# Optimization experiments

Measured on AMD Instinct MI355X. Metric: run time of the kernel, lower is better.

The kernel has to match this reference:

```python
import jax, jax.numpy as jnp
import numpy as np

EPS = 1e-5
K = 3

def _bn(x, g, b):
    # training-mode BatchNorm2d: batch stats over (N,H,W), biased variance
    m = jnp.mean(x, axis=(0, 2, 3), keepdims=True)
    v = jnp.var(x, axis=(0, 2, 3), keepdims=True)
    return (x - m) * jax.lax.rsqrt(v + EPS) * g[None, :, None, None] + b[None, :, None, None]

def _gelu(x):
    return jax.nn.gelu(x, approximate=False)

def _dyn_dw(x, aw1, ab1, aw2, ab2):
    # dynamic depthwise conv: per-sample k^2 softmax weights shared over channels
    b, c, h, w = x.shape
    gap = jnp.mean(x, axis=(2, 3))                              # (b,c)
    h1 = jax.nn.relu(jnp.einsum('oc,bc->bo', aw1, gap) + ab1)   # (b,c//8)
    kw = jax.nn.softmax(jnp.einsum('oc,bc->bo', aw2, h1) + ab2, axis=1)  # (b,k^2)
    xp = jnp.pad(x, ((0, 0), (0, 0), (1, 1), (1, 1)))
    out = jnp.zeros_like(x)
    idx = 0
    for i in range(K):
        for j in range(K):
            out = out + kw[:, idx, None, None, None] * xp[:, :, i:i + h, j:j + w]
            idx += 1
    return out

def _channel_att(x, w1, w2):
    avg = jnp.mean(x, axis=(2, 3))        # (b,C)
    mx = jnp.max(x, axis=(2, 3))          # (b,C)
    def fc(v):
        return jnp.einsum('oc,bc->bo', w2, jax.nn.relu(jnp.einsum('oc,bc->bo', w1, v)))
    s = jax.nn.sigmoid(fc(avg) + fc(mx))  # (b,C)
    return s[:, :, None, None] * x

def _forward(x, w1, b1, g1, be1, aw1, ab1, aw2, ab2, g2, be2,
             ca_w1, ca_w2, pw, pb, g3, be3, sw, sb):
    b, n, d = x.shape
    h = w = int(np.sqrt(n))
    residual = x
    xi = jnp.transpose(x.reshape(b, h, w, d), (0, 3, 1, 2))       # (b,d,h,w)
    # pw_expand: 1x1 conv -> GELU -> BN
    y = jnp.einsum('oc,bchw->bohw', w1, xi) + b1[None, :, None, None]
    y = _bn(_gelu(y), g1, be1)                                    # (b,4d,h,w)
    # dw_conv: dynamic depthwise -> GELU -> BN -> channel attention
    y = _dyn_dw(y, aw1, ab1, aw2, ab2)
    y = _bn(_gelu(y), g2, be2)
    y = _channel_att(y, ca_w1, ca_w2)
    # spatial attention
    avg_o = jnp.mean(y, axis=1, keepdims=True)
    max_o = jnp.max(y, axis=1, keepdims=True)
    sp_in = jnp.concatenate([avg_o, max_o], axis=1)               # (b,2,h,w)
    sp = jax.lax.conv_general_dilated(sp_in, sw, (1, 1), ((3, 3), (3, 3)),
                                      dimension_numbers=('NCHW', 'OIHW', 'NCHW'))
    sp = jax.nn.sigmoid(sp + sb[None, :, None, None])
    y = y * sp
    # pw_project: 1x1 conv -> BN
    y = jnp.einsum('oc,bchw->bohw', pw, y) + pb[None, :, None, None]
    y = _bn(y, g3, be3)
    y = jnp.transpose(y, (0, 2, 3, 1)).reshape(b, n, d)
    return residual + y

def setup_inputs() -> dict:
    key = jax.random.key(0)
    ks = jax.random.split(key, 16)
    d, C = 256, 1024
    def rn(k, shape, fan):
        return jax.random.normal(k, shape, jnp.float32) * np.float32(np.sqrt(2.0 / fan))
    return {
        'x': jax.random.normal(ks[0], (8, 1024, d), jnp.float32),
        'w1': rn(ks[1], (C, d), d), 'b1': jnp.zeros((C,), jnp.float32),
        'g1': jnp.ones((C,), jnp.float32), 'be1': jnp.zeros((C,), jnp.float32),
        'aw1': rn(ks[2], (C // 8, C), C), 'ab1': jnp.zeros((C // 8,), jnp.float32),
        'aw2': rn(ks[3], (K * K, C // 8), C // 8), 'ab2': jnp.zeros((K * K,), jnp.float32),
        'g2': jnp.ones((C,), jnp.float32), 'be2': jnp.zeros((C,), jnp.float32),
        'ca_w1': rn(ks[4], (C // 16, C), C), 'ca_w2': rn(ks[5], (C, C // 16), C // 16),
        'pw': rn(ks[6], (d, C), C), 'pb': jnp.zeros((d,), jnp.float32),
        'g3': jnp.ones((d,), jnp.float32), 'be3': jnp.zeros((d,), jnp.float32),
        'sw': rn(ks[7], (1, 2, 7, 7), 2 * 49), 'sb': jnp.zeros((1,), jnp.float32),
    }

def reference(x, w1, b1, g1, be1, aw1, ab1, aw2, ab2, g2, be2,
              ca_w1, ca_w2, pw, pb, g3, be3, sw, sb):
    return _forward(x, w1, b1, g1, be1, aw1, ab1, aw2, ab2, g2, be2,
                    ca_w1, ca_w2, pw, pb, g3, be3, sw, sb)
```

## Files before the change

kernel.cpp:

```cpp
#include <hip/hip_runtime.h>
#include <math.h>

constexpr int B = 8;
constexpr int D = 256;
constexpr int C = 1024;
constexpr int H = 32, W = 32;
constexpr int P = H * W;
constexpr int M = B * P;
constexpr float EPS = 1e-5f;

typedef unsigned short u16;
typedef unsigned int u32;
typedef __attribute__((ext_vector_type(8))) short short8;
typedef __attribute__((ext_vector_type(4))) float floatx4;

constexpr size_t WS_CHSUM1 = 0;
constexpr size_t WS_CHSQ1  = 1024;
constexpr size_t WS_GAPSUM = 2048;
constexpr size_t WS_CHSUM3 = 10240;
constexpr size_t WS_CHSQ3  = 10496;
constexpr size_t WS_ACC_COUNT = 10752;
constexpr size_t WS_SCALE1 = 11264;
constexpr size_t WS_SHIFT1 = 12288;
constexpr size_t WS_KW     = 21504;
constexpr size_t WS_SCALE2 = 21760;
constexpr size_t WS_SHIFT2 = 22784;
constexpr size_t WS_AVGBN  = 23808;
constexpr size_t WS_MXBN   = 32000;
constexpr size_t WS_SATT   = 40192;
constexpr size_t WS_AVGO   = 48384;
constexpr size_t WS_MAXO   = 56576;
constexpr size_t WS_SP     = 64768;
constexpr size_t WS_PSUM2  = 73728;
constexpr size_t WS_PSQ2   = 335872;
constexpr size_t WS_PMAX2  = 598016;
constexpr size_t WS_PMIN2  = 860160;
constexpr size_t WS_PRE    = 1122304;
constexpr size_t WS_T1B    = 3219456;
constexpr size_t WS_T2B    = 7413760;
constexpr size_t WS_XB     = 11608064;
constexpr size_t WS_W1B    = 12656640;
constexpr size_t WS_PWB    = 12787712;
constexpr size_t WS_YB     = 12918784;

__device__ __forceinline__ float gelu_exact(float v) {
    return 0.5f * v * (1.0f + erff(v * 0.70710678118654752440f));
}

__device__ __forceinline__ u16 f2bf(float f) {
    u32 u = __float_as_uint(f);
    u += 0x7fff + ((u >> 16) & 1);
    return (u16)(u >> 16);
}

__device__ __forceinline__ float bf2f(u16 v) {
    return __uint_as_float(((u32)v) << 16);
}

__global__ __launch_bounds__(256) void cvt_all_kernel(const float* __restrict__ x,
                                                      const float* __restrict__ w1,
                                                      const float* __restrict__ pw,
                                                      u16* __restrict__ xb,
                                                      u16* __restrict__ w1b,
                                                      u16* __restrict__ pwb) {
    const int i = blockIdx.x * 256 + threadIdx.x;
    const float* src;
    u16* dst;
    int off;
    if (i < 524288)      { src = x;  dst = xb;  off = i; }
    else if (i < 589824) { src = w1; dst = w1b; off = i - 524288; }
    else                 { src = pw; dst = pwb; off = i - 589824; }
    const float4 v = *(const float4*)(src + (size_t)off * 4);
    uint2 o;
    o.x = ((u32)f2bf(v.x)) | ((u32)f2bf(v.y) << 16);
    o.y = ((u32)f2bf(v.z)) | ((u32)f2bf(v.w) << 16);
    *(uint2*)(dst + (size_t)off * 4) = o;
}

template<int KD, int EPI, int NS, int MB, int NB>
__global__ __launch_bounds__(256) void mfma_gemm_kernel(
    const u16* __restrict__ A,
    const u16* __restrict__ Bw,
    const float* __restrict__ bias,
    const float* __restrict__ rowscale,
    void* __restrict__ outv,
    float* __restrict__ csum,
    float* __restrict__ csq,
    float* __restrict__ gsum)
{
    constexpr int MI = MB / 32;
    constexpr int NJ = NB / 32;
    extern __shared__ u16 smem[];
    u16* As = smem;
    u16* Bs = smem + MB * 32;
    const int t = threadIdx.x;
    const int lane = t & 63;
    const int row0 = blockIdx.y * MB;
    const int col0 = blockIdx.x * NB;
    const int wv = t >> 6;
    const int wrow = (wv >> 1) * (MB / 2);
    const int wcol = (wv & 1) * (NB / 2);
    const int lm = lane & 15;
    const int lk8 = (lane >> 4) * 8;

    const int srow = t >> 2;
    const int scol = (t & 3) * 8;

    const u16* gA0 = A + (size_t)(row0 + srow) * KD + scol;
    const u16* gA1 = A + (size_t)(row0 + 64 + srow) * KD + scol;
    const u16* gB0 = Bw + (size_t)(col0 + srow) * KD + scol;

    const floatx4 zero = {0.f, 0.f, 0.f, 0.f};
    floatx4 acc[MI][NJ];
#pragma unroll
    for (int i = 0; i < MI; ++i)
#pragma unroll
        for (int j = 0; j < NJ; ++j) acc[i][j] = zero;

    for (int k0 = 0; k0 < KD; k0 += 32) {
        __builtin_amdgcn_global_load_lds(
            (const __attribute__((address_space(1))) void*)(gA0 + k0),
            (__attribute__((address_space(3))) void*)(As + t * 8), 16, 0, 0);
        if (MB == 128)
            __builtin_amdgcn_global_load_lds(
                (const __attribute__((address_space(1))) void*)(gA1 + k0),
                (__attribute__((address_space(3))) void*)(As + 2048 + t * 8), 16, 0, 0);
        __builtin_amdgcn_global_load_lds(
            (const __attribute__((address_space(1))) void*)(gB0 + k0),
            (__attribute__((address_space(3))) void*)(Bs + t * 8), 16, 0, 0);
        __syncthreads();
        short8 af[MI], bf[NJ];
#pragma unroll
        for (int i = 0; i < MI; ++i)
            af[i] = *(const short8*)(As + (wrow + i * 16 + lm) * 32 + lk8);
#pragma unroll
        for (int j = 0; j < NJ; ++j)
            bf[j] = *(const short8*)(Bs + (wcol + j * 16 + lm) * 32 + lk8);
#pragma unroll
        for (int i = 0; i < MI; ++i)
#pragma unroll
            for (int j = 0; j < NJ; ++j)
                acc[i][j] = __builtin_amdgcn_mfma_f32_16x16x32_bf16(af[i], bf[j], acc[i][j], 0, 0, 0);
        __syncthreads();
    }

    float colsum[NJ], colsq[NJ];
#pragma unroll
    for (int j = 0; j < NJ; ++j) { colsum[j] = 0.f; colsq[j] = 0.f; }

    if (EPI == 0) {
        u16* Cs = smem;
#pragma unroll
        for (int i = 0; i < MI; ++i) {
#pragma unroll
            for (int r = 0; r < 4; ++r) {
                const int lrow = wrow + i * 16 + (lane >> 4) * 4 + r;
#pragma unroll
                for (int j = 0; j < NJ; ++j) {
                    const int lcol = wcol + j * 16 + lm;
                    const float tv = gelu_exact(acc[i][j][r] + bias[col0 + lcol]);
                    Cs[lrow * NB + lcol] = f2bf(tv);
                    colsum[j] += tv;
                    colsq[j] = fmaf(tv, tv, colsq[j]);
                }
            }
        }
        __syncthreads();
        const int rr = t >> 1;
        const int hh = (t & 1) * 32;
        u16* outp = (u16*)outv + (size_t)(row0 + rr) * NS + col0 + hh;
#pragma unroll
        for (int k = 0; k < 4; ++k) {
            *(uint4*)(outp + k * 8) = *(const uint4*)(Cs + rr * NB + hh + k * 8);
        }
    } else {
#pragma unroll
        for (int i = 0; i < MI; ++i) {
#pragma unroll
            for (int r = 0; r < 4; ++r) {
                const int grow = row0 + wrow + i * 16 + (lane >> 4) * 4 + r;
                const float rs = rowscale[grow];
#pragma unroll
                for (int j = 0; j < NJ; ++j) {
                    const int gcol = col0 + wcol + j * 16 + lm;
                    const float tv = rs * acc[i][j][r] + bias[gcol];
                    ((float*)outv)[(size_t)grow * NS + gcol] = tv;
                    colsum[j] += tv;
                    colsq[j] = fmaf(tv, tv, colsq[j]);
                }
            }
        }
    }

    const int bb = (blockIdx.y * MB) >> 10;
#pragma unroll
    for (int j = 0; j < NJ; ++j) {
        float s = colsum[j];
        float q = colsq[j];
        s += __shfl_xor(s, 16); s += __shfl_xor(s, 32);
        q += __shfl_xor(q, 16); q += __shfl_xor(q, 32);
        if (lane < 16) {
            const int c = col0 + wcol + j * 16 + lm;
            atomicAdd(&csum[c], s);
            atomicAdd(&csq[c], q);
            if (EPI == 0) atomicAdd(&gsum[bb * NS + c], s);
        }
    }
}

__global__ __launch_bounds__(1024) void dynmlp_kernel(const float* __restrict__ chsum1,
                                                      const float* __restrict__ chsq1,
                                                      const float* __restrict__ gapsum,
                                                      const float* __restrict__ g1,
                                                      const float* __restrict__ be1,
                                                      const float* __restrict__ aw1,
                                                      const float* __restrict__ ab1,
                                                      const float* __restrict__ aw2,
                                                      const float* __restrict__ ab2,
                                                      float* __restrict__ scale1,
                                                      float* __restrict__ shift1,
                                                      float* __restrict__ kw) {
    const int b = blockIdx.x;
    const int t = threadIdx.x;
    const int wave = t >> 6, lane = t & 63;
    __shared__ float g[1024];
    __shared__ float h1[128];
    __shared__ float logits[12];
    {
        const float m = chsum1[t] * (1.0f / (float)M);
        const float var = chsq1[t] * (1.0f / (float)M) - m * m;
        const float rstd = rsqrtf(var + EPS);
        const float sc = rstd * g1[t];
        const float sh = be1[t] - m * sc;
        if (b == 0) { scale1[t] = sc; shift1[t] = sh; }
        g[t] = gapsum[b * C + t] * (1.0f / (float)P) * sc + sh;
    }
    __syncthreads();
#pragma unroll
    for (int k = 0; k < 8; ++k) {
        const int u = wave * 8 + k;
        const float4* wr = (const float4*)(aw1 + (size_t)u * C);
        float s = 0.f;
#pragma unroll
        for (int ch = 0; ch < 4; ++ch) {
            const float4 wv = wr[lane + 64 * ch];
            const float4 sv = *(const float4*)(g + 4 * lane + 256 * ch);
            s += wv.x * sv.x + wv.y * sv.y + wv.z * sv.z + wv.w * sv.w;
        }
#pragma unroll
        for (int off = 1; off < 64; off <<= 1) s += __shfl_xor(s, off);
        if (lane == 0) h1[u] = fmaxf(s + ab1[u], 0.f);
    }
    __syncthreads();
    if (wave < 9) {
        float s = aw2[wave * 128 + lane] * h1[lane]
                + aw2[wave * 128 + 64 + lane] * h1[64 + lane];
#pragma unroll
        for (int off = 1; off < 64; off <<= 1) s += __shfl_xor(s, off);
        if (lane == 0) logits[wave] = s + ab2[wave];
    }
    __syncthreads();
    if (t == 0) {
        float mx = logits[0];
        for (int i = 1; i < 9; ++i) mx = fmaxf(mx, logits[i]);
        float e[9], den = 0.f;
        for (int i = 0; i < 9; ++i) { e[i] = expf(logits[i] - mx); den += e[i]; }
        const float inv = 1.0f / den;
        for (int i = 0; i < 9; ++i) kw[b * 9 + i] = e[i] * inv;
    }
}

__global__ __launch_bounds__(256) void dwconv_kernel(const u16* __restrict__ t1b,
                                                     const float* __restrict__ scale1,
                                                     const float* __restrict__ shift1,
                                                     const float* __restrict__ kw,
                                                     u16* __restrict__ t2b,
                                                     float* __restrict__ psum,
                                                     float* __restrict__ psq,
                                                     float* __restrict__ pmax,
                                                     float* __restrict__ pmin) {
    const int b = blockIdx.y >> 5;
    const int h = blockIdx.y & 31;
    const int c0 = (blockIdx.x * 256 + threadIdx.x) * 2;
    float k[9];
#pragma unroll
    for (int i = 0; i < 9; ++i) k[i] = kw[b * 9 + i];
    const float sc0 = scale1[c0],     sh0 = shift1[c0];
    const float sc1 = scale1[c0 + 1], sh1 = shift1[c0 + 1];
    const u16* base = t1b + (size_t)b * P * C + c0;
    const bool rok[3] = { h > 0, true, h < H - 1 };

    float2 win[3][3];
    const float2 z = {0.f, 0.f};
#pragma unroll
    for (int ri = 0; ri < 3; ++ri) {
        win[ri][0] = z;
#pragma unroll
        for (int ci = 1; ci < 3; ++ci) {
            if (rok[ri]) {
                const u32 v = *(const u32*)(base + ((size_t)((h + ri - 1) * W + (ci - 1))) * C);
                float2 r;
                r.x = fmaf(bf2f((u16)(v & 0xffff)), sc0, sh0);
                r.y = fmaf(bf2f((u16)(v >> 16)),    sc1, sh1);
                win[ri][ci] = r;
            } else win[ri][ci] = z;
        }
    }

    float s0 = 0.f, q0 = 0.f, mx0 = -INFINITY, mn0 = INFINITY;
    float s1 = 0.f, q1 = 0.f, mx1 = -INFINITY, mn1 = INFINITY;
    for (int w = 0; w < W; ++w) {
        float a0 = 0.f, a1 = 0.f;
#pragma unroll
        for (int ri = 0; ri < 3; ++ri)
#pragma unroll
            for (int ci = 0; ci < 3; ++ci) {
                a0 = fmaf(k[ri * 3 + ci], win[ri][ci].x, a0);
                a1 = fmaf(k[ri * 3 + ci], win[ri][ci].y, a1);
            }
        const float y0 = gelu_exact(a0);
        const float y1 = gelu_exact(a1);
        *(u32*)(t2b + ((size_t)b * P + h * W + w) * C + c0) =
            ((u32)f2bf(y0)) | ((u32)f2bf(y1) << 16);
        s0 += y0; q0 = fmaf(y0, y0, q0); mx0 = fmaxf(mx0, y0); mn0 = fminf(mn0, y0);
        s1 += y1; q1 = fmaf(y1, y1, q1); mx1 = fmaxf(mx1, y1); mn1 = fminf(mn1, y1);
        if (w < W - 1) {
#pragma unroll
            for (int ri = 0; ri < 3; ++ri) {
                win[ri][0] = win[ri][1];
                win[ri][1] = win[ri][2];
                if (rok[ri] && (w + 2 < W)) {
                    const u32 v = *(const u32*)(base + ((size_t)((h + ri - 1) * W + (w + 2))) * C);
                    float2 r;
                    r.x = fmaf(bf2f((u16)(v & 0xffff)), sc0, sh0);
                    r.y = fmaf(bf2f((u16)(v >> 16)),    sc1, sh1);
                    win[ri][2] = r;
                } else win[ri][2] = z;
            }
        }
    }
    const int idx = b * 32 + h;
    psum[c0 * 256 + idx] = s0;  psum[(c0 + 1) * 256 + idx] = s1;
    psq [c0 * 256 + idx] = q0;  psq [(c0 + 1) * 256 + idx] = q1;
    pmax[c0 * 256 + idx] = mx0; pmax[(c0 + 1) * 256 + idx] = mx1;
    pmin[c0 * 256 + idx] = mn0; pmin[(c0 + 1) * 256 + idx] = mn1;
}

__global__ __launch_bounds__(256) void stats2_kernel(const float* __restrict__ psum,
                                                     const float* __restrict__ psq,
                                                     const float* __restrict__ pmax,
                                                     const float* __restrict__ pmin,
                                                     const float* __restrict__ g2,
                                                     const float* __restrict__ be2,
                                                     float* __restrict__ scale2,
                                                     float* __restrict__ shift2,
                                                     float* __restrict__ avgbn,
                                                     float* __restrict__ mxbn) {
    const int c = blockIdx.x;
    const int t = threadIdx.x;
    const int base = c * 256 + t;
    float s  = psum[base];
    float q  = psq[base];
    float mx = pmax[base];
    float mn = pmin[base];
#pragma unroll
    for (int off = 1; off < 32; off <<= 1) {
        s += __shfl_xor(s, off);
        q += __shfl_xor(q, off);
        mx = fmaxf(mx, __shfl_xor(mx, off));
        mn = fminf(mn, __shfl_xor(mn, off));
    }
    __shared__ float bs[8], bq[8], bmx[8], bmn[8];
    __shared__ float sc_sh[2];
    if ((t & 31) == 0) {
        const int b = t >> 5;
        bs[b] = s; bq[b] = q; bmx[b] = mx; bmn[b] = mn;
    }
    __syncthreads();
    if (t == 0) {
        float S = 0.f, Q = 0.f;
#pragma unroll
        for (int b = 0; b < 8; ++b) { S += bs[b]; Q += bq[b]; }
        const float m = S * (1.0f / (float)M);
        const float var = Q * (1.0f / (float)M) - m * m;
        const float rstd = rsqrtf(var + EPS);
        const float sc = rstd * g2[c];
        const float sh = be2[c] - m * sc;
        scale2[c] = sc;
        shift2[c] = sh;
        sc_sh[0] = sc; sc_sh[1] = sh;
    }
    __syncthreads();
    if (t < 8) {
        const float sc = sc_sh[0], sh = sc_sh[1];
        avgbn[t * C + c] = bs[t] * (1.0f / (float)P) * sc + sh;
        mxbn[t * C + c] = (sc >= 0.f ? bmx[t] : bmn[t]) * sc + sh;
    }
}

__global__ __launch_bounds__(1024) void chatt_kernel(const float* __restrict__ avgbn,
                                                     const float* __restrict__ mxbn,
                                                     const float* __restrict__ caw1,
                                                     const float* __restrict__ caw2,
                                                     float* __restrict__ s_att) {
    const int b = blockIdx.x;
    const int t = threadIdx.x;
    const int wave = t >> 6, lane = t & 63;
    __shared__ float la[1024], lx[1024], ha[64], hm[64];
    la[t] = avgbn[b * C + t];
    lx[t] = mxbn[b * C + t];
    __syncthreads();
#pragma unroll
    for (int k = 0; k < 8; ++k) {
        const int u = wave * 8 + k;
        const int row = u & 63;
        const float* src = (u < 64) ? la : lx;
        const float4* wr = (const float4*)(caw1 + (size_t)row * C);
        float s = 0.f;
#pragma unroll
        for (int ch = 0; ch < 4; ++ch) {
            const float4 wv = wr[lane + 64 * ch];
            const float4 sv = *(const float4*)(src + 4 * lane + 256 * ch);
            s += wv.x * sv.x + wv.y * sv.y + wv.z * sv.z + wv.w * sv.w;
        }
#pragma unroll
        for (int off = 1; off < 64; off <<= 1) s += __shfl_xor(s, off);
        if (lane == 0) {
            s = fmaxf(s, 0.f);
            if (u < 64) ha[row] = s; else hm[row] = s;
        }
    }
    __syncthreads();
    {
        const float4* w2 = (const float4*)(caw2 + (size_t)t * 64);
        float s = 0.f;
#pragma unroll
        for (int j = 0; j < 16; ++j) {
            const float4 wv = w2[j];
            s += wv.x * (ha[j * 4 + 0] + hm[j * 4 + 0]);
            s += wv.y * (ha[j * 4 + 1] + hm[j * 4 + 1]);
            s += wv.z * (ha[j * 4 + 2] + hm[j * 4 + 2]);
            s += wv.w * (ha[j * 4 + 3] + hm[j * 4 + 3]);
        }
        s_att[b * C + t] = 1.0f / (1.0f + expf(-s));
    }
}

__global__ __launch_bounds__(256) void yq_kernel(const u16* __restrict__ t2b,
                                                 const float* __restrict__ scale2,
                                                 const float* __restrict__ shift2,
                                                 const float* __restrict__ s_att,
                                                 u16* __restrict__ yb,
                                                 float* __restrict__ avg_o,
                                                 float* __restrict__ max_o) {
    const int row = blockIdx.x;
    const int b = row >> 10;
    const int t = threadIdx.x;
    const int c0 = t * 4;
    const uint2 vv = *(const uint2*)(t2b + (size_t)row * C + c0);
    const float v0 = bf2f((u16)(vv.x & 0xffff));
    const float v1 = bf2f((u16)(vv.x >> 16));
    const float v2 = bf2f((u16)(vv.y & 0xffff));
    const float v3 = bf2f((u16)(vv.y >> 16));
    const float4 sc = *(const float4*)(scale2 + c0);
    const float4 sh = *(const float4*)(shift2 + c0);
    const float4 sa = *(const float4*)(s_att + (size_t)b * C + c0);
    const float y0 = fmaf(v0, sc.x, sh.x) * sa.x;
    const float y1 = fmaf(v1, sc.y, sh.y) * sa.y;
    const float y2 = fmaf(v2, sc.z, sh.z) * sa.z;
    const float y3 = fmaf(v3, sc.w, sh.w) * sa.w;
    uint2 o;
    o.x = ((u32)f2bf(y0)) | ((u32)f2bf(y1) << 16);
    o.y = ((u32)f2bf(y2)) | ((u32)f2bf(y3) << 16);
    *(uint2*)(yb + (size_t)row * C + c0) = o;
    float s = (y0 + y1) + (y2 + y3);
    float mx = fmaxf(fmaxf(y0, y1), fmaxf(y2, y3));
#pragma unroll
    for (int off = 32; off > 0; off >>= 1) {
        s += __shfl_down(s, off);
        mx = fmaxf(mx, __shfl_down(mx, off));
    }
    __shared__ float ss[4], sm[4];
    const int wave = t >> 6, lane = t & 63;
    if (lane == 0) { ss[wave] = s; sm[wave] = mx; }
    __syncthreads();
    if (t == 0) {
        const float S = ss[0] + ss[1] + ss[2] + ss[3];
        const float Mx = fmaxf(fmaxf(sm[0], sm[1]), fmaxf(sm[2], sm[3]));
        avg_o[row] = S * (1.0f / (float)C);
        max_o[row] = Mx;
    }
}

__global__ __launch_bounds__(1024) void spconv_kernel(const float* __restrict__ avg_o,
                                                      const float* __restrict__ max_o,
                                                      const float* __restrict__ sw,
                                                      const float* __restrict__ sb,
                                                      float* __restrict__ sp) {
    const int b = blockIdx.x;
    const int t = threadIdx.x;
    __shared__ float pa[P], pm[P], wsh[98];
    pa[t] = avg_o[b * P + t];
    pm[t] = max_o[b * P + t];
    if (t < 98) wsh[t] = sw[t];
    const float sbv = sb[0];
    __syncthreads();
    const int h = t >> 5, w = t & 31;
    float acc = sbv;
#pragma unroll
    for (int i = 0; i < 7; ++i) {
        const int hh = h + i - 3;
        if (hh < 0 || hh >= H) continue;
#pragma unroll
        for (int j = 0; j < 7; ++j) {
            const int ww = w + j - 3;
            if (ww < 0 || ww >= W) continue;
            const int pidx = hh * W + ww;
            acc = fmaf(wsh[i * 7 + j], pa[pidx], acc);
            acc = fmaf(wsh[49 + i * 7 + j], pm[pidx], acc);
        }
    }
    sp[b * P + t] = 1.0f / (1.0f + expf(-acc));
}

__global__ __launch_bounds__(256) void final_kernel(const float* __restrict__ x,
                                                    const float* __restrict__ pre,
                                                    const float* __restrict__ chsum3,
                                                    const float* __restrict__ chsq3,
                                                    const float* __restrict__ g3,
                                                    const float* __restrict__ be3,
                                                    float* __restrict__ out) {
    __shared__ float lsc[256], lsh[256];
    const int t = threadIdx.x;
    {
        const float m = chsum3[t] * (1.0f / (float)M);
        const float var = chsq3[t] * (1.0f / (float)M) - m * m;
        const float rstd = rsqrtf(var + EPS);
        const float sc = rstd * g3[t];
        lsc[t] = sc;
        lsh[t] = be3[t] - m * sc;
    }
    __syncthreads();
    const int i = blockIdx.x * 256 + t;
    const int e = i * 4;
    const int d = e & 255;
    const float4 xv = *(const float4*)(x + e);
    const float4 pv = *(const float4*)(pre + e);
    const float4 sc = *(const float4*)(lsc + d);
    const float4 sh = *(const float4*)(lsh + d);
    float4 o;
    o.x = xv.x + fmaf(pv.x, sc.x, sh.x);
    o.y = xv.y + fmaf(pv.y, sc.y, sh.y);
    o.z = xv.z + fmaf(pv.z, sc.z, sh.z);
    o.w = xv.w + fmaf(pv.w, sc.w, sh.w);
    *(float4*)(out + e) = o;
}

extern "C" void kernel_launch(void* const* d_in, const int* in_sizes, int n_in,
                              void* d_out, int out_size, void* d_ws, size_t ws_size,
                              hipStream_t stream) {
    const float* x    = (const float*)d_in[0];
    const float* w1   = (const float*)d_in[1];
    const float* b1   = (const float*)d_in[2];
    const float* g1   = (const float*)d_in[3];
    const float* be1  = (const float*)d_in[4];
    const float* aw1  = (const float*)d_in[5];
    const float* ab1  = (const float*)d_in[6];
    const float* aw2  = (const float*)d_in[7];
    const float* ab2  = (const float*)d_in[8];
    const float* g2   = (const float*)d_in[9];
    const float* be2  = (const float*)d_in[10];
    const float* caw1 = (const float*)d_in[11];
    const float* caw2 = (const float*)d_in[12];
    const float* pw   = (const float*)d_in[13];
    const float* pb   = (const float*)d_in[14];
    const float* g3   = (const float*)d_in[15];
    const float* be3  = (const float*)d_in[16];
    const float* sw   = (const float*)d_in[17];
    const float* sb   = (const float*)d_in[18];
    float* out = (float*)d_out;
    float* ws = (float*)d_ws;

    hipMemsetAsync(ws, 0, WS_ACC_COUNT * sizeof(float), stream);

    float* chsum1  = ws + WS_CHSUM1;
    float* chsq1   = ws + WS_CHSQ1;
    float* gapsum  = ws + WS_GAPSUM;
    float* chsum3  = ws + WS_CHSUM3;
    float* chsq3   = ws + WS_CHSQ3;
    float* scale1  = ws + WS_SCALE1;
    float* shift1  = ws + WS_SHIFT1;
    float* kw      = ws + WS_KW;
    float* scale2  = ws + WS_SCALE2;
    float* shift2  = ws + WS_SHIFT2;
    float* avgbn   = ws + WS_AVGBN;
    float* mxbn    = ws + WS_MXBN;
    float* s_att   = ws + WS_SATT;
    float* avg_o   = ws + WS_AVGO;
    float* max_o   = ws + WS_MAXO;
    float* sp      = ws + WS_SP;
    float* psum2   = ws + WS_PSUM2;
    float* psq2    = ws + WS_PSQ2;
    float* pmax2   = ws + WS_PMAX2;
    float* pmin2   = ws + WS_PMIN2;
    float* pre     = ws + WS_PRE;
    u16* t1b = (u16*)(ws + WS_T1B);
    u16* t2b = (u16*)(ws + WS_T2B);
    u16* xb  = (u16*)(ws + WS_XB);
    u16* w1b = (u16*)(ws + WS_W1B);
    u16* pwb = (u16*)(ws + WS_PWB);
    u16* yb  = (u16*)(ws + WS_YB);

    cvt_all_kernel<<<dim3(2560), 256, 0, stream>>>(x, w1, pw, xb, w1b, pwb);
    mfma_gemm_kernel<256, 0, C, 128, 64><<<dim3(C / 64, M / 128), 256, 16384, stream>>>(
        xb, w1b, b1, nullptr, t1b, chsum1, chsq1, gapsum);
    dynmlp_kernel<<<dim3(B), 1024, 0, stream>>>(chsum1, chsq1, gapsum, g1, be1,
                                                aw1, ab1, aw2, ab2, scale1, shift1, kw);
    dwconv_kernel<<<dim3(C / 512, B * H), 256, 0, stream>>>(t1b, scale1, shift1, kw, t2b,
                                                            psum2, psq2, pmax2, pmin2);
    stats2_kernel<<<dim3(C), 256, 0, stream>>>(psum2, psq2, pmax2, pmin2, g2, be2,
                                               scale2, shift2, avgbn, mxbn);
    chatt_kernel<<<dim3(B), 1024, 0, stream>>>(avgbn, mxbn, caw1, caw2, s_att);
    yq_kernel<<<dim3(M), 256, 0, stream>>>(t2b, scale2, shift2, s_att, yb, avg_o, max_o);
    spconv_kernel<<<dim3(B), 1024, 0, stream>>>(avg_o, max_o, sw, sb, sp);
    mfma_gemm_kernel<1024, 1, D, 64, 64><<<dim3(D / 64, M / 64), 256, 8192, stream>>>(
        yb, pwb, pb, sp, pre, chsum3, chsq3, nullptr);
    final_kernel<<<dim3((M * D / 4) / 256), 256, 0, stream>>>(x, pre, chsum3, chsq3, g3, be3, out);
}
```

Before: 218.9 us.

## Fuse the whole pipeline into one persistent cooperative kernel with grid syncs

Adds a single cooperative mega-kernel of 512 blocks x 256 threads. It runs every stage in sequence, separated by grid-wide barriers: zeroing the workspace, bf16 conversion, the expand GEMM with GELU and statistics, the dynamic-weight MLP, the depthwise conv, BN2 finalisation, channel attention, the spatial reductions, the 7x7 conv, the projection GEMM, and the final BN plus residual. The aim is to remove per-kernel launch overhead, the separate memset and the gaps between the roughly ten kernels. In exchange, the small per-batch stages run on only 8 blocks while the rest of the grid waits, each grid.sync adds barrier latency, and the fixed grid size limits occupancy. The old multi-kernel path is kept as a fallback if the cooperative launch fails.

Result: slower. 808.0 us (+269.1%).

```diff
diff --git a/kernel.cpp b/kernel.cpp
--- a/kernel.cpp
+++ b/kernel.cpp
@@ -1,5 +1,8 @@
 #include <hip/hip_runtime.h>
+#include <hip/hip_cooperative_groups.h>
 #include <math.h>
+
+namespace cg = cooperative_groups;
 
 constexpr int B = 8;
 constexpr int D = 256;
@@ -57,6 +60,563 @@
     return __uint_as_float(((u32)v) << 16);
 }
 
+constexpr int NBLK = 512;
+constexpr int NTHR = 256;
+
+struct MegaParams {
+    const float *x, *w1, *b1, *g1, *be1, *aw1, *ab1, *aw2, *ab2, *g2, *be2,
+                *caw1, *caw2, *pw, *pb, *g3, *be3, *sw, *sb;
+    float* out;
+    float* ws;
+};
+
+__global__ __launch_bounds__(256, 2) void mega_kernel(MegaParams p) {
+    __shared__ __align__(16) u16 smu[8256];
+    float* smf = (float*)smu;
+
+    float* ws = p.ws;
+    float* chsum1 = ws + WS_CHSUM1;
+    float* chsq1  = ws + WS_CHSQ1;
+    float* gapsum = ws + WS_GAPSUM;
+    float* chsum3 = ws + WS_CHSUM3;
+    float* chsq3  = ws + WS_CHSQ3;
+    float* scale1 = ws + WS_SCALE1;
+    float* shift1 = ws + WS_SHIFT1;
+    float* kw     = ws + WS_KW;
+    float* scale2 = ws + WS_SCALE2;
+    float* shift2 = ws + WS_SHIFT2;
+    float* avgbn  = ws + WS_AVGBN;
+    float* mxbn   = ws + WS_MXBN;
+    float* s_att  = ws + WS_SATT;
+    float* avg_o  = ws + WS_AVGO;
+    float* max_o  = ws + WS_MAXO;
+    float* sp     = ws + WS_SP;
+    float* psum   = ws + WS_PSUM2;
+    float* psq    = ws + WS_PSQ2;
+    float* pmax   = ws + WS_PMAX2;
+    float* pmin   = ws + WS_PMIN2;
+    float* pre    = ws + WS_PRE;
+    u16* t1b = (u16*)(ws + WS_T1B);
+    u16* t2b = (u16*)(ws + WS_T2B);
+    u16* xb  = (u16*)(ws + WS_XB);
+    u16* w1b = (u16*)(ws + WS_W1B);
+    u16* pwb = (u16*)(ws + WS_PWB);
+    u16* yb  = (u16*)(ws + WS_YB);
+
+    cg::grid_group grid = cg::this_grid();
+    const int bid = blockIdx.x;
+    const int t = threadIdx.x;
+    const int lane = t & 63;
+    const int wave = t >> 6;
+    const int gtid = bid * NTHR + t;
+
+    for (int i = gtid; i < (int)WS_ACC_COUNT; i += NBLK * NTHR) ws[i] = 0.f;
+    for (int u = gtid; u < 655360; u += NBLK * NTHR) {
+        const float* src; u16* dst; int off;
+        if (u < 524288)      { src = p.x;  dst = xb;  off = u; }
+        else if (u < 589824) { src = p.w1; dst = w1b; off = u - 524288; }
+        else                 { src = p.pw; dst = pwb; off = u - 589824; }
+        const float4 v = *(const float4*)(src + (size_t)off * 4);
+        uint2 o;
+        o.x = ((u32)f2bf(v.x)) | ((u32)f2bf(v.y) << 16);
+        o.y = ((u32)f2bf(v.z)) | ((u32)f2bf(v.w) << 16);
+        *(uint2*)(dst + (size_t)off * 4) = o;
+    }
+    grid.sync();
+
+    {
+        u16* As = smu;
+        u16* Bs = smu + 4096;
+        u16* Cs = smu;
+        const int wrow = (wave >> 1) * 64;
+        const int wcol = (wave & 1) * 32;
+        const int lm = lane & 15;
+        const int lk8 = (lane >> 4) * 8;
+        const int srow = t >> 2;
+        const int scol = (t & 3) * 8;
+        for (int tile = bid; tile < 1024; tile += NBLK) {
+            const int row0 = (tile >> 4) * 128;
+            const int col0 = (tile & 15) * 64;
+            const u16* gA0 = xb + (size_t)(row0 + srow) * 256 + scol;
+            const u16* gA1 = xb + (size_t)(row0 + 64 + srow) * 256 + scol;
+            const u16* gB0 = w1b + (size_t)(col0 + srow) * 256 + scol;
+            const floatx4 zero = {0.f, 0.f, 0.f, 0.f};
+            floatx4 acc[4][2];
+#pragma unroll
+            for (int i = 0; i < 4; ++i) { acc[i][0] = zero; acc[i][1] = zero; }
+            for (int k0 = 0; k0 < 256; k0 += 32) {
+                __builtin_amdgcn_global_load_lds(
+                    (const __attribute__((address_space(1))) void*)(gA0 + k0),
+                    (__attribute__((address_space(3))) void*)(As + t * 8), 16, 0, 0);
+                __builtin_amdgcn_global_load_lds(
+                    (const __attribute__((address_space(1))) void*)(gA1 + k0),
+                    (__attribute__((address_space(3))) void*)(As + 2048 + t * 8), 16, 0, 0);
+                __builtin_amdgcn_global_load_lds(
+                    (const __attribute__((address_space(1))) void*)(gB0 + k0),
+                    (__attribute__((address_space(3))) void*)(Bs + t * 8), 16, 0, 0);
+                __syncthreads();
+                short8 af[4], bf[2];
+#pragma unroll
+                for (int i = 0; i < 4; ++i)
+                    af[i] = *(const short8*)(As + (wrow + i * 16 + lm) * 32 + lk8);
+#pragma unroll
+                for (int j = 0; j < 2; ++j)
+                    bf[j] = *(const short8*)(Bs + (wcol + j * 16 + lm) * 32 + lk8);
+#pragma unroll
+                for (int i = 0; i < 4; ++i)
+#pragma unroll
+                    for (int j = 0; j < 2; ++j)
+                        acc[i][j] = __builtin_amdgcn_mfma_f32_16x16x32_bf16(af[i], bf[j], acc[i][j], 0, 0, 0);
+                __syncthreads();
+            }
+            float colsum[2] = {0.f, 0.f}, colsq[2] = {0.f, 0.f};
+#pragma unroll
+            for (int i = 0; i < 4; ++i) {
+#pragma unroll
+                for (int r = 0; r < 4; ++r) {
+                    const int lrow = wrow + i * 16 + (lane >> 4) * 4 + r;
+#pragma unroll
+                    for (int j = 0; j < 2; ++j) {
+                        const int lcol = wcol + j * 16 + lm;
+                        const float tv = gelu_exact(acc[i][j][r] + p.b1[col0 + lcol]);
+                        Cs[lrow * 64 + lcol] = f2bf(tv);
+                        colsum[j] += tv;
+                        colsq[j] = fmaf(tv, tv, colsq[j]);
+                    }
+                }
+            }
+            __syncthreads();
+            {
+                const int rr = t >> 1;
+                const int hh = (t & 1) * 32;
+                u16* outp = t1b + (size_t)(row0 + rr) * C + col0 + hh;
+#pragma unroll
+                for (int k = 0; k < 4; ++k)
+                    *(uint4*)(outp + k * 8) = *(const uint4*)(Cs + rr * 64 + hh + k * 8);
+            }
+            const int bb = row0 >> 10;
+#pragma unroll
+            for (int j = 0; j < 2; ++j) {
+                float s = colsum[j];
+                float q = colsq[j];
+                s += __shfl_xor(s, 16); s += __shfl_xor(s, 32);
+                q += __shfl_xor(q, 16); q += __shfl_xor(q, 32);
+                if (lane < 16) {
+                    const int c = col0 + wcol + j * 16 + lm;
+                    atomicAdd(&chsum1[c], s);
+                    atomicAdd(&chsq1[c], q);
+                    atomicAdd(&gapsum[bb * C + c], s);
+                }
+            }
+            __syncthreads();
+        }
+    }
+    grid.sync();
+
+    if (bid < 8) {
+        const int b = bid;
+        float* g = smf;
+        float* h1 = smf + 1024;
+        float* logits = smf + 1152;
+#pragma unroll
+        for (int cc = 0; cc < 4; ++cc) {
+            const int c = t + 256 * cc;
+            const float m = chsum1[c] * (1.0f / (float)M);
+            const float var = chsq1[c] * (1.0f / (float)M) - m * m;
+            const float rstd = rsqrtf(var + EPS);
+            const float sc = rstd * p.g1[c];
+            const float sh = p.be1[c] - m * sc;
+            if (b == 0) { scale1[c] = sc; shift1[c] = sh; }
+            g[c] = gapsum[b * C + c] * (1.0f / (float)P) * sc + sh;
+        }
+        __syncthreads();
+        for (int k = 0; k < 32; ++k) {
+            const int u = wave * 32 + k;
+            const float4* wr = (const float4*)(p.aw1 + (size_t)u * C);
+            float s = 0.f;
+#pragma unroll
+            for (int ch = 0; ch < 4; ++ch) {
+                const float4 wv = wr[lane + 64 * ch];
+                const float4 sv = *(const float4*)(g + 4 * lane + 256 * ch);
+                s += wv.x * sv.x + wv.y * sv.y + wv.z * sv.z + wv.w * sv.w;
+            }
+#pragma unroll
+            for (int off = 1; off < 64; off <<= 1) s += __shfl_xor(s, off);
+            if (lane == 0) h1[u] = fmaxf(s + p.ab1[u], 0.f);
+        }
+        __syncthreads();
+        if (t < 9) {
+            float s = p.ab2[t];
+            for (int j = 0; j < 128; ++j) s = fmaf(p.aw2[t * 128 + j], h1[j], s);
+            logits[t] = s;
+        }
+        __syncthreads();
+        if (t == 0) {
+            float mx = logits[0];
+            for (int i = 1; i < 9; ++i) mx = fmaxf(mx, logits[i]);
+            float e[9], den = 0.f;
+            for (int i = 0; i < 9; ++i) { e[i] = expf(logits[i] - mx); den += e[i]; }
+            const float inv = 1.0f / den;
+            for (int i = 0; i < 9; ++i) kw[b * 9 + i] = e[i] * inv;
+        }
+    }
+    grid.sync();
+
+    {
+        const int cb = bid & 1;
+        const int bh = bid >> 1;
+        const int b = bh >> 5;
+        const int h = bh & 31;
+        const int c0 = (cb * 256 + t) * 2;
+        float k[9];
+#pragma unroll
+        for (int i = 0; i < 9; ++i) k[i] = kw[b * 9 + i];
+        const float sc0 = scale1[c0],     sh0 = shift1[c0];
+        const float sc1 = scale1[c0 + 1], sh1 = shift1[c0 + 1];
+        const u16* base = t1b + (size_t)b * P * C + c0;
+        const bool rok[3] = { h > 0, true, h < H - 1 };
+        float2 win[3][3];
+        const float2 z = {0.f, 0.f};
+#pragma unroll
+        for (int ri = 0; ri < 3; ++ri) {
+            win[ri][0] = z;
+#pragma unroll
+            for (int ci = 1; ci < 3; ++ci) {
+                if (rok[ri]) {
+                    const u32 v = *(const u32*)(base + ((size_t)((h + ri - 1) * W + (ci - 1))) * C);
+                    float2 r;
+                    r.x = fmaf(bf2f((u16)(v & 0xffff)), sc0, sh0);
+                    r.y = fmaf(bf2f((u16)(v >> 16)),    sc1, sh1);
+                    win[ri][ci] = r;
+                } else win[ri][ci] = z;
+            }
+        }
+        float s0 = 0.f, q0 = 0.f, mx0 = -INFINITY, mn0 = INFINITY;
+        float s1 = 0.f, q1 = 0.f, mx1 = -INFINITY, mn1 = INFINITY;
+        for (int w = 0; w < W; ++w) {
+            float a0 = 0.f, a1 = 0.f;
+#pragma unroll
+            for (int ri = 0; ri < 3; ++ri)
+#pragma unroll
+                for (int ci = 0; ci < 3; ++ci) {
+                    a0 = fmaf(k[ri * 3 + ci], win[ri][ci].x, a0);
+                    a1 = fmaf(k[ri * 3 + ci], win[ri][ci].y, a1);
+                }
+            const float y0 = gelu_exact(a0);
+            const float y1 = gelu_exact(a1);
+            *(u32*)(t2b + ((size_t)b * P + h * W + w) * C + c0) =
+                ((u32)f2bf(y0)) | ((u32)f2bf(y1) << 16);
+            s0 += y0; q0 = fmaf(y0, y0, q0); mx0 = fmaxf(mx0, y0); mn0 = fminf(mn0, y0);
+            s1 += y1; q1 = fmaf(y1, y1, q1); mx1 = fmaxf(mx1, y1); mn1 = fminf(mn1, y1);
+            if (w < W - 1) {
+#pragma unroll
+                for (int ri = 0; ri < 3; ++ri) {
+                    win[ri][0] = win[ri][1];
+                    win[ri][1] = win[ri][2];
+                    if (rok[ri] && (w + 2 < W)) {
+                        const u32 v = *(const u32*)(base + ((size_t)((h + ri - 1) * W + (w + 2))) * C);
+                        float2 r;
+                        r.x = fmaf(bf2f((u16)(v & 0xffff)), sc0, sh0);
+                        r.y = fmaf(bf2f((u16)(v >> 16)),    sc1, sh1);
+                        win[ri][2] = r;
+                    } else win[ri][2] = z;
+                }
+            }
+        }
+        const int idx = b * 32 + h;
+        psum[c0 * 256 + idx] = s0;  psum[(c0 + 1) * 256 + idx] = s1;
+        psq [c0 * 256 + idx] = q0;  psq [(c0 + 1) * 256 + idx] = q1;
+        pmax[c0 * 256 + idx] = mx0; pmax[(c0 + 1) * 256 + idx] = mx1;
+        pmin[c0 * 256 + idx] = mn0; pmin[(c0 + 1) * 256 + idx] = mn1;
+    }
+    grid.sync();
+
+    {
+        float* bs = smf;
+        float* bq = smf + 8;
+        float* bmx = smf + 16;
+        float* bmn = smf + 24;
+        float* sc_sh = smf + 32;
+        for (int c = bid; c < C; c += NBLK) {
+            const int base = c * 256 + t;
+            float s  = psum[base];
+            float q  = psq[base];
+            float mx = pmax[base];
+            float mn = pmin[base];
+#pragma unroll
+            for (int off = 1; off < 32; off <<= 1) {
+                s += __shfl_xor(s, off);
+                q += __shfl_xor(q, off);
+                mx = fmaxf(mx, __shfl_xor(mx, off));
+                mn = fminf(mn, __shfl_xor(mn, off));
+            }
+            if ((t & 31) == 0) {
+                const int b = t >> 5;
+                bs[b] = s; bq[b] = q; bmx[b] = mx; bmn[b] = mn;
+            }
+            __syncthreads();
+            if (t == 0) {
+                float S = 0.f, Q = 0.f;
+#pragma unroll
+                for (int b = 0; b < 8; ++b) { S += bs[b]; Q += bq[b]; }
+                const float m = S * (1.0f / (float)M);
+                const float var = Q * (1.0f / (float)M) - m * m;
+                const float rstd = rsqrtf(var + EPS);
+                const float sc = rstd * p.g2[c];
+                const float sh = p.be2[c] - m * sc;
+                scale2[c] = sc;
+                shift2[c] = sh;
+                sc_sh[0] = sc; sc_sh[1] = sh;
+            }
+            __syncthreads();
+            if (t < 8) {
+                const float sc = sc_sh[0], sh = sc_sh[1];
+                avgbn[t * C + c] = bs[t] * (1.0f / (float)P) * sc + sh;
+                mxbn[t * C + c] = (sc >= 0.f ? bmx[t] : bmn[t]) * sc + sh;
+            }
+            __syncthreads();
+        }
+    }
+    grid.sync();
+
+    if (bid < 8) {
+        const int b = bid;
+        float* la = smf;
+        float* lx = smf + 1024;
+        float* ha = smf + 2048;
+        float* hm = smf + 2112;
+#pragma unroll
+        for (int cc = 0; cc < 4; ++cc) {
+            const int c = t + 256 * cc;
+            la[c] = avgbn[b * C + c];
+            lx[c] = mxbn[b * C + c];
+        }
+        __syncthreads();
+        for (int k = 0; k < 32; ++k) {
+            const int u = wave * 32 + k;
+            const int row = u & 63;
+            const float* src = (u < 64) ? la : lx;
+            const float4* wr = (const float4*)(p.caw1 + (size_t)row * C);
+            float s = 0.f;
+#pragma unroll
+            for (int ch = 0; ch < 4; ++ch) {
+                const float4 wv = wr[lane + 64 * ch];
+                const float4 sv = *(const float4*)(src + 4 * lane + 256 * ch);
+                s += wv.x * sv.x + wv.y * sv.y + wv.z * sv.z + wv.w * sv.w;
+            }
+#pragma unroll
+            for (int off = 1; off < 64; off <<= 1) s += __shfl_xor(s, off);
+            if (lane == 0) {
+                s = fmaxf(s, 0.f);
+                if (u < 64) ha[row] = s; else hm[row] = s;
+            }
+        }
+        __syncthreads();
+#pragma unroll
+        for (int cc = 0; cc < 4; ++cc) {
+            const int c = t + 256 * cc;
+            const float4* w2 = (const float4*)(p.caw2 + (size_t)c * 64);
+            float s = 0.f;
+#pragma unroll
+            for (int j = 0; j < 16; ++j) {
+                const float4 wv = w2[j];
+                s += wv.x * (ha[j * 4 + 0] + hm[j * 4 + 0]);
+                s += wv.y * (ha[j * 4 + 1] + hm[j * 4 + 1]);
+                s += wv.z * (ha[j * 4 + 2] + hm[j * 4 + 2]);
+                s += wv.w * (ha[j * 4 + 3] + hm[j * 4 + 3]);
+            }
+            s_att[b * C + c] = 1.0f / (1.0f + expf(-s));
+        }
+    }
+    grid.sync();
+
+    {
+        const int gw = bid * 4 + wave;
+        for (int row = gw; row < M; row += NBLK * 4) {
+            const int b = row >> 10;
+            float s = 0.f, mx = -INFINITY;
+#pragma unroll
+            for (int cc = 0; cc < 4; ++cc) {
+                const int c0 = lane * 4 + 256 * cc;
+                const uint2 vv = *(const uint2*)(t2b + (size_t)row * C + c0);
+                const float v0 = bf2f((u16)(vv.x & 0xffff));
+                const float v1 = bf2f((u16)(vv.x >> 16));
+                const float v2 = bf2f((u16)(vv.y & 0xffff));
+                const float v3 = bf2f((u16)(vv.y >> 16));
+                const float4 sc = *(const float4*)(scale2 + c0);
+                const float4 sh = *(const float4*)(shift2 + c0);
+                const float4 sa = *(const float4*)(s_att + (size_t)b * C + c0);
+                const float y0 = fmaf(v0, sc.x, sh.x) * sa.x;
+                const float y1 = fmaf(v1, sc.y, sh.y) * sa.y;
+                const float y2 = fmaf(v2, sc.z, sh.z) * sa.z;
+                const float y3 = fmaf(v3, sc.w, sh.w) * sa.w;
+                uint2 o;
+                o.x = ((u32)f2bf(y0)) | ((u32)f2bf(y1) << 16);
+                o.y = ((u32)f2bf(y2)) | ((u32)f2bf(y3) << 16);
+                *(uint2*)(yb + (size_t)row * C + c0) = o;
+                s += (y0 + y1) + (y2 + y3);
+                mx = fmaxf(mx, fmaxf(fmaxf(y0, y1), fmaxf(y2, y3)));
+            }
+#pragma unroll
+            for (int off = 1; off < 64; off <<= 1) {
+                s += __shfl_xor(s, off);
+                mx = fmaxf(mx, __shfl_xor(mx, off));
+            }
+            if (lane == 0) {
+                avg_o[row] = s * (1.0f / (float)C);
+                max_o[row] = mx;
+            }
+        }
+    }
+    grid.sync();
+
+    if (bid < 8) {
+        const int b = bid;
+        float* pa = smf;
+        float* pm = smf + 1024;
+        float* wsh = smf + 2048;
+#pragma unroll
+        for (int cc = 0; cc < 4; ++cc) {
+            const int i = t + 256 * cc;
+            pa[i] = avg_o[b * P + i];
+            pm[i] = max_o[b * P + i];
+        }
+        if (t < 98) wsh[t] = p.sw[t];
+        const float sbv = p.sb[0];
+        __syncthreads();
+#pragma unroll
+        for (int cc = 0; cc < 4; ++cc) {
+            const int idx = t + 256 * cc;
+            const int h = idx >> 5, w = idx & 31;
+            float acc = sbv;
+#pragma unroll
+            for (int i = 0; i < 7; ++i) {
+                const int hh = h + i - 3;
+                if (hh < 0 || hh >= H) continue;
+#pragma unroll
+                for (int j = 0; j < 7; ++j) {
+                    const int ww = w + j - 3;
+                    if (ww < 0 || ww >= W) continue;
+                    const int pidx = hh * W + ww;
+                    acc = fmaf(wsh[i * 7 + j], pa[pidx], acc);
+                    acc = fmaf(wsh[49 + i * 7 + j], pm[pidx], acc);
+                }
+            }
+            sp[b * P + idx] = 1.0f / (1.0f + expf(-acc));
+        }
+    }
+    grid.sync();
+
+    {
+        u16* As = smu;
+        u16* Bs = smu + 2048;
+        float* Cs = smf;
+        const int wrow = (wave >> 1) * 32;
+        const int wcol = (wave & 1) * 32;
+        const int lm = lane & 15;
+        const int lk8 = (lane >> 4) * 8;
+        const int srow = t >> 2;
+        const int scol = (t & 3) * 8;
+        const int row0 = (bid >> 2) * 64;
+        const int col0 = (bid & 3) * 64;
+        const u16* gA0 = yb + (size_t)(row0 + srow) * C + scol;
+        const u16* gB0 = pwb + (size_t)(col0 + srow) * C + scol;
+        const floatx4 zero = {0.f, 0.f, 0.f, 0.f};
+        floatx4 acc[2][2];
+        acc[0][0] = zero; acc[0][1] = zero; acc[1][0] = zero; acc[1][1] = zero;
+        for (int k0 = 0; k0 < C; k0 += 32) {
+            __builtin_amdgcn_global_load_lds(
+                (const __attribute__((address_space(1))) void*)(gA0 + k0),
+                (__attribute__((address_space(3))) void*)(As + t * 8), 16, 0, 0);
+            __builtin_amdgcn_global_load_lds(
+                (const __attribute__((address_space(1))) void*)(gB0 + k0),
+                (__attribute__((address_space(3))) void*)(Bs + t * 8), 16, 0, 0);
+            __syncthreads();
+            short8 af[2], bf[2];
+#pragma unroll
+            for (int i = 0; i < 2; ++i)
+                af[i] = *(const short8*)(As + (wrow + i * 16 + lm) * 32 + lk8);
+#pragma unroll
+            for (int j = 0; j < 2; ++j)
+                bf[j] = *(const short8*)(Bs + (wcol + j * 16 + lm) * 32 + lk8);
+#pragma unroll
+            for (int i = 0; i < 2; ++i)
+#pragma unroll
+                for (int j = 0; j < 2; ++j)
+                    acc[i][j] = __builtin_amdgcn_mfma_f32_16x16x32_bf16(af[i], bf[j], acc[i][j], 0, 0, 0);
+            __syncthreads();
+        }
+        float colsum[2] = {0.f, 0.f}, colsq[2] = {0.f, 0.f};
+#pragma unroll
+        for (int i = 0; i < 2; ++i) {
+#pragma unroll
+            for (int r = 0; r < 4; ++r) {
+                const int lrow = wrow + i * 16 + (lane >> 4) * 4 + r;
+                const float rs = sp[row0 + lrow];
+#pragma unroll
+                for (int j = 0; j < 2; ++j) {
+                    const int lcol = wcol + j * 16 + lm;
+                    const float tv = rs * acc[i][j][r] + p.pb[col0 + lcol];
+                    Cs[lrow * 64 + lcol] = tv;
+                    colsum[j] += tv;
+                    colsq[j] = fmaf(tv, tv, colsq[j]);
+                }
+            }
+        }
+        __syncthreads();
+        {
+            const int rr = t >> 2;
+            const int hh = (t & 3) * 16;
+            float* outp = pre + (size_t)(row0 + rr) * D + col0 + hh;
+#pragma unroll
+            for (int k = 0; k < 4; ++k)
+                *(float4*)(outp + k * 4) = *(const float4*)(Cs + rr * 64 + hh + k * 4);
+        }
+#pragma unroll
+        for (int j = 0; j < 2; ++j) {
+            float s = colsum[j];
+            float q = colsq[j];
+            s += __shfl_xor(s, 16); s += __shfl_xor(s, 32);
+            q += __shfl_xor(q, 16); q += __shfl_xor(q, 32);
+            if (lane < 16) {
+                const int c = col0 + wcol + j * 16 + lm;
+                atomicAdd(&chsum3[c], s);
+                atomicAdd(&chsq3[c], q);
+            }
+        }
+    }
+    grid.sync();
+
+    {
+        float* lsc = smf;
+        float* lsh = smf + 256;
+        {
+            const float m = chsum3[t] * (1.0f / (float)M);
+            const float var = chsq3[t] * (1.0f / (float)M) - m * m;
+            const float rstd = rsqrtf(var + EPS);
+            const float sc = rstd * p.g3[t];
+            lsc[t] = sc;
+            lsh[t] = p.be3[t] - m * sc;
+        }
+        __syncthreads();
+        for (int i = gtid; i < M * D / 4; i += NBLK * NTHR) {
+            const int e = i * 4;
+            const int d = e & 255;
+            const float4 xv = *(const float4*)(p.x + e);
+            const float4 pv = *(const float4*)(pre + e);
+            const float4 sc = *(const float4*)(lsc + d);
+            const float4 sh = *(const float4*)(lsh + d);
+            float4 o;
+            o.x = xv.x + fmaf(pv.x, sc.x, sh.x);
+            o.y = xv.y + fmaf(pv.y, sc.y, sh.y);
+            o.z = xv.z + fmaf(pv.z, sc.z, sh.z);
+            o.w = xv.w + fmaf(pv.w, sc.w, sh.w);
+            *(float4*)(p.out + e) = o;
+        }
+    }
+}
+
+
 __global__ __launch_bounds__(256) void cvt_all_kernel(const float* __restrict__ x,
                                                       const float* __restrict__ w1,
                                                       const float* __restrict__ pw,
@@ -102,21 +662,17 @@
     const int wcol = (wv & 1) * (NB / 2);
     const int lm = lane & 15;
     const int lk8 = (lane >> 4) * 8;
-
     const int srow = t >> 2;
     const int scol = (t & 3) * 8;
-
     const u16* gA0 = A + (size_t)(row0 + srow) * KD + scol;
     const u16* gA1 = A + (size_t)(row0 + 64 + srow) * KD + scol;
     const u16* gB0 = Bw + (size_t)(col0 + srow) * KD + scol;
-
     const floatx4 zero = {0.f, 0.f, 0.f, 0.f};
     floatx4 acc[MI][NJ];
 #pragma unroll
     for (int i = 0; i < MI; ++i)
 #pragma unroll
         for (int j = 0; j < NJ; ++j) acc[i][j] = zero;
-
     for (int k0 = 0; k0 < KD; k0 += 32) {
         __builtin_amdgcn_global_load_lds(
             (const __attribute__((address_space(1))) void*)(gA0 + k0),
@@ -143,11 +699,9 @@
                 acc[i][j] = __builtin_amdgcn_mfma_f32_16x16x32_bf16(af[i], bf[j], acc[i][j], 0, 0, 0);
         __syncthreads();
     }
-
     float colsum[NJ], colsq[NJ];
 #pragma unroll
     for (int j = 0; j < NJ; ++j) { colsum[j] = 0.f; colsq[j] = 0.f; }
-
     if (EPI == 0) {
         u16* Cs = smem;
 #pragma unroll
@@ -191,7 +745,6 @@
             }
         }
     }
-
     const int bb = (blockIdx.y * MB) >> 10;
 #pragma unroll
     for (int j = 0; j < NJ; ++j) {
@@ -289,7 +842,6 @@
     const float sc1 = scale1[c0 + 1], sh1 = shift1[c0 + 1];
     const u16* base = t1b + (size_t)b * P * C + c0;
     const bool rok[3] = { h > 0, true, h < H - 1 };
-
     float2 win[3][3];
     const float2 z = {0.f, 0.f};
 #pragma unroll
@@ -306,7 +858,6 @@
             } else win[ri][ci] = z;
         }
     }
-
     float s0 = 0.f, q0 = 0.f, mx0 = -INFINITY, mn0 = INFINITY;
     float s1 = 0.f, q1 = 0.f, mx1 = -INFINITY, mn1 = INFINITY;
     for (int w = 0; w < W; ++w) {
@@ -581,8 +1132,19 @@
     float* out = (float*)d_out;
     float* ws = (float*)d_ws;
 
+    MegaParams mp;
+    mp.x = x; mp.w1 = w1; mp.b1 = b1; mp.g1 = g1; mp.be1 = be1;
+    mp.aw1 = aw1; mp.ab1 = ab1; mp.aw2 = aw2; mp.ab2 = ab2;
+    mp.g2 = g2; mp.be2 = be2; mp.caw1 = caw1; mp.caw2 = caw2;
+    mp.pw = pw; mp.pb = pb; mp.g3 = g3; mp.be3 = be3; mp.sw = sw; mp.sb = sb;
+    mp.out = out; mp.ws = ws;
+    void* kargs[] = { (void*)&mp };
+    hipError_t err = hipLaunchCooperativeKernel((const void*)mega_kernel,
+                                                dim3(NBLK), dim3(NTHR), kargs, 0, stream);
+    if (err == hipSuccess) return;
+    (void)hipGetLastError();
+
     hipMemsetAsync(ws, 0, WS_ACC_COUNT * sizeof(float), stream);
-
     float* chsum1  = ws + WS_CHSUM1;
     float* chsq1   = ws + WS_CHSQ1;
     float* gapsum  = ws + WS_GAPSUM;
```
